# Optimization experiments

Hardware: AMD Instinct MI355X
Metric: run time of the kernel (lower is better)

Reference implementation:

```python
import jax, jax.numpy as jnp
import numpy as np

LN_EPS = 1e-5

def _ln(x, g, b):
    mu = x.mean(-1, keepdims=True)
    var = ((x - mu) ** 2).mean(-1, keepdims=True)
    return (x - mu) * jax.lax.rsqrt(var + LN_EPS) * g + b

def _gru(x, h, wih, whh, bih, bhh):
    # torch GRUCell: gates ordered (r, z, n)
    gi = x @ wih.T + bih
    gh = h @ whh.T + bhh
    ir, iz, inn = jnp.split(gi, 3, axis=-1)
    hr, hz, hn = jnp.split(gh, 3, axis=-1)
    r = jax.nn.sigmoid(ir + hr)
    z = jax.nn.sigmoid(iz + hz)
    n = jnp.tanh(inn + r * hn)
    return (1.0 - z) * n + z * h

def setup_inputs() -> dict:
    key = jax.random.key(0)
    ks = jax.random.split(key, 10)
    B, N, D, S, H = 64, 4096, 128, 8, 256
    w = D ** -0.5  # weight scale to keep activations sane
    return {
        'inputs': jax.random.normal(ks[0], (B, N, D), jnp.float32),
        'slot_noise': jax.random.normal(ks[1], (1, S, D), jnp.float32),
        'slots_mu': jax.random.normal(ks[2], (1, S, D), jnp.float32) * w,
        'slots_log_sigma': jnp.zeros((1, S, D), jnp.float32),
        'wq': jax.random.normal(ks[3], (D, D), jnp.float32) * w,
        'bq': jnp.zeros((D,), jnp.float32),
        'wk': jax.random.normal(ks[4], (D, D), jnp.float32) * w,
        'bk': jnp.zeros((D,), jnp.float32),
        'wv': jax.random.normal(ks[5], (D, D), jnp.float32) * w,
        'bv': jnp.zeros((D,), jnp.float32),
        'gru_wih': jax.random.normal(ks[6], (3 * D, D), jnp.float32) * w,
        'gru_whh': jax.random.normal(ks[7], (3 * D, D), jnp.float32) * w,
        'gru_bih': jnp.zeros((3 * D,), jnp.float32),
        'gru_bhh': jnp.zeros((3 * D,), jnp.float32),
        'ns_g': jnp.ones((D,), jnp.float32),
        'ns_b': jnp.zeros((D,), jnp.float32),
        'ni_g': jnp.ones((D,), jnp.float32),
        'ni_b': jnp.zeros((D,), jnp.float32),
        'mlp_ln_g': jnp.ones((D,), jnp.float32),
        'mlp_ln_b': jnp.zeros((D,), jnp.float32),
        'mlp_w1': jax.random.normal(ks[8], (H, D), jnp.float32) * w,
        'mlp_b1': jnp.zeros((H,), jnp.float32),
        'mlp_w2': jax.random.normal(ks[9], (D, H), jnp.float32) * (H ** -0.5),
        'mlp_b2': jnp.zeros((D,), jnp.float32),
    }

N_ITERS = 3

def reference(inputs, slot_noise, slots_mu, slots_log_sigma, wq, bq, wk, bk, wv, bv,
              gru_wih, gru_whh, gru_bih, gru_bhh, ns_g, ns_b, ni_g, ni_b,
              mlp_ln_g, mlp_ln_b, mlp_w1, mlp_b1, mlp_w2, mlp_b2):
    B, N, D = inputs.shape
    S = slots_mu.shape[1]
    slots = slots_mu + jnp.exp(slots_log_sigma) * slot_noise  # [1,S,D]
    slots = jnp.broadcast_to(slots, (B, S, D))
    x = _ln(inputs, ni_g, ni_b)
    k = x @ wk.T + bk  # [B,N,D]
    v = x @ wv.T + bv
    scale = 1.0 / jnp.sqrt(jnp.float32(D))
    for _ in range(N_ITERS):
        q = _ln(slots, ns_g, ns_b) @ wq.T + bq  # [B,S,D]
        logits = jnp.einsum('bnd,bsd->bns', k, q) * scale
        attn = jax.nn.softmax(logits, axis=-1)  # softmax over slots
        attn_norm = jnp.clip(attn.sum(axis=1, keepdims=True), 1e-8, None)
        slot_attn = attn / attn_norm
        updates = jnp.einsum('bns,bnd->bsd', slot_attn, v)
        slots = _gru(updates, slots, gru_wih, gru_whh, gru_bih, gru_bhh)
        h = jax.nn.gelu(_ln(slots, mlp_ln_g, mlp_ln_b) @ mlp_w1.T + mlp_b1, approximate=False)
        slots = slots + (h @ mlp_w2.T + mlp_b2)
    return slots
```

## Files before the change

kernel.cpp:

```cpp
#include <hip/hip_runtime.h>
#include <hip/hip_bf16.h>
#include <math.h>

#define Bn 64
#define Nn 4096
#define Dn 128
#define Sn 8
#define Hn 256
#define LN_EPS 1e-5f
#define QSCALE 0.08838834764831845f
#define NCHUNK 16

typedef __bf16 bf16x8 __attribute__((ext_vector_type(8)));
typedef float f32x4 __attribute__((ext_vector_type(4)));
typedef unsigned short ushort_t;

__device__ __forceinline__ float dot4(float4 a, float4 b) {
    return a.x*b.x + a.y*b.y + a.z*b.z + a.w*b.w;
}
__device__ __forceinline__ ushort_t f2bf(float f) {
    __bf16 b = (__bf16)f;
    ushort_t u; __builtin_memcpy(&u, &b, 2); return u;
}
__device__ __forceinline__ bf16x8 zero8() {
    bf16x8 z;
    #pragma unroll
    for (int i = 0; i < 8; ++i) z[i] = (__bf16)0.0f;
    return z;
}

__global__ void k_prep(const float* __restrict__ wk, const float* __restrict__ wv,
                       ushort_t* __restrict__ wallT,
                       const float* __restrict__ mu, const float* __restrict__ ls,
                       const float* __restrict__ noise, float* __restrict__ slots) {
    if (blockIdx.x < 128) {
        int o = blockIdx.x * 256 + threadIdx.x;
        int e = o & 7;
        int l = (o >> 3) & 15;
        int q = (o >> 7) & 3;
        int k = (o >> 9) & 3;
        int G = o >> 11;
        int row = G * 16 + l;
        int col = k * 32 + q * 8 + e;
        float f = (row < 128) ? wk[row * 128 + col] : wv[(row - 128) * 128 + col];
        wallT[o] = f2bf(f);
    } else {
        int i = (blockIdx.x - 128) * 256 + threadIdx.x;
        if (i < Sn * Dn) {
            float v = mu[i] + __expf(ls[i]) * noise[i];
            #pragma unroll 4
            for (int b = 0; b < Bn; ++b) slots[b * Sn * Dn + i] = v;
        }
    }
}

__global__ __launch_bounds__(512) void k_lnkv_mfma(
    const float* __restrict__ inp, const float* __restrict__ ni_g, const float* __restrict__ ni_b,
    const ushort_t* __restrict__ wallT, const float* __restrict__ bk, const float* __restrict__ bv,
    ushort_t* __restrict__ kout, ushort_t* __restrict__ vout)
{
    __shared__ ushort_t wsh[32768];
    const int t = threadIdx.x;
    const int lane = t & 63;
    const int w = t >> 6;
    const int l15 = lane & 15, q = lane >> 4;
    const int rowbase = blockIdx.x * 128;
    const int row = rowbase + w * 16 + l15;
    const int b_idx = rowbase >> 12;

    const float* xr = inp + (size_t)row * Dn + q * 8;
    float4 xv[8];
    #pragma unroll
    for (int c = 0; c < 4; ++c) {
        xv[2*c]   = *(const float4*)(xr + c * 32);
        xv[2*c+1] = *(const float4*)(xr + c * 32 + 4);
    }
    #pragma unroll
    for (int i = 0; i < 8; ++i) {
        int off = (i * 512 + t) * 8;
        *(bf16x8*)&wsh[off] = *(const bf16x8*)&wallT[off];
    }

    float s = 0.f, sq = 0.f;
    #pragma unroll
    for (int i = 0; i < 8; ++i) {
        float4 x4 = xv[i];
        s  += x4.x + x4.y + x4.z + x4.w;
        sq += x4.x*x4.x + x4.y*x4.y + x4.z*x4.z + x4.w*x4.w;
    }
    s  += __shfl_xor(s, 16);  s  += __shfl_xor(s, 32);
    sq += __shfl_xor(sq, 16); sq += __shfl_xor(sq, 32);
    float mu = s * (1.0f / 128.0f);
    float rs = rsqrtf(sq * (1.0f / 128.0f) - mu * mu + LN_EPS);

    bf16x8 xf[4];
    #pragma unroll
    for (int c = 0; c < 4; ++c) {
        const float* gp = ni_g + c * 32 + q * 8;
        const float* bp = ni_b + c * 32 + q * 8;
        float4 g0 = *(const float4*)gp, g1 = *(const float4*)(gp + 4);
        float4 b0 = *(const float4*)bp, b1 = *(const float4*)(bp + 4);
        bf16x8 f;
        f[0] = (__bf16)((xv[2*c].x   - mu) * rs * g0.x + b0.x);
        f[1] = (__bf16)((xv[2*c].y   - mu) * rs * g0.y + b0.y);
        f[2] = (__bf16)((xv[2*c].z   - mu) * rs * g0.z + b0.z);
        f[3] = (__bf16)((xv[2*c].w   - mu) * rs * g0.w + b0.w);
        f[4] = (__bf16)((xv[2*c+1].x - mu) * rs * g1.x + b1.x);
        f[5] = (__bf16)((xv[2*c+1].y - mu) * rs * g1.y + b1.y);
        f[6] = (__bf16)((xv[2*c+1].z - mu) * rs * g1.z + b1.z);
        f[7] = (__bf16)((xv[2*c+1].w - mu) * rs * g1.w + b1.w);
        xf[c] = f;
    }

    __syncthreads();

    const int nloc0 = (rowbase & 4095) + w * 16 + q * 4;
    #pragma unroll
    for (int ct = 0; ct < 16; ++ct) {
        bf16x8 af[4];
        #pragma unroll
        for (int k4 = 0; k4 < 4; ++k4)
            af[k4] = *(const bf16x8*)&wsh[((ct * 4 + k4) * 64 + lane) * 8];
        f32x4 acc = {0.f, 0.f, 0.f, 0.f};
        if (ct < 8) {
            #pragma unroll
            for (int k4 = 0; k4 < 4; ++k4)
                acc = __builtin_amdgcn_mfma_f32_16x16x32_bf16(af[k4], xf[k4], acc, 0, 0, 0);
            int d0 = ct * 16 + q * 4;
            float4 bia = *(const float4*)&bk[d0];
            ushort4 o = { f2bf(acc[0] + bia.x), f2bf(acc[1] + bia.y),
                          f2bf(acc[2] + bia.z), f2bf(acc[3] + bia.w) };
            size_t off = ((size_t)(((rowbase >> 4) + w) * 4 + (d0 >> 5)) * 64
                          + ((d0 >> 3) & 3) * 16 + l15) * 8 + (d0 & 7);
            *(ushort4*)&kout[off] = o;
        } else {
            #pragma unroll
            for (int k4 = 0; k4 < 4; ++k4)
                acc = __builtin_amdgcn_mfma_f32_16x16x32_bf16(xf[k4], af[k4], acc, 0, 0, 0);
            int dgrp = ct - 8;
            float bb = bv[dgrp * 16 + l15];
            ushort4 o = { f2bf(acc[0] + bb), f2bf(acc[1] + bb),
                          f2bf(acc[2] + bb), f2bf(acc[3] + bb) };
            size_t off = (((size_t)(b_idx * 8 + dgrp) * 128 + (nloc0 >> 5)) * 64
                          + ((nloc0 >> 3) & 3) * 16 + l15) * 8 + (nloc0 & 7);
            *(ushort4*)&vout[off] = o;
        }
    }
}

__global__ __launch_bounds__(256) void k_qproj2(
    const float* __restrict__ slots, const float* __restrict__ ns_g, const float* __restrict__ ns_b,
    const float* __restrict__ wq, const float* __restrict__ bq,
    ushort_t* __restrict__ qb)
{
    __shared__ float lnq[8][128];
    const int t = threadIdx.x;
    const int bs0 = blockIdx.x * 8;
    {
        int r = t >> 5, c = (t & 31) * 4;
        float4 x4 = *(const float4*)&slots[(size_t)(bs0 + r) * Dn + c];
        float s  = x4.x + x4.y + x4.z + x4.w;
        float sq = x4.x*x4.x + x4.y*x4.y + x4.z*x4.z + x4.w*x4.w;
        #pragma unroll
        for (int m = 1; m <= 16; m <<= 1) { s += __shfl_xor(s, m); sq += __shfl_xor(sq, m); }
        float mu = s * (1.0f / 128.0f);
        float rs = rsqrtf(sq * (1.0f / 128.0f) - mu * mu + LN_EPS);
        lnq[r][c+0] = (x4.x - mu) * rs * ns_g[c+0] + ns_b[c+0];
        lnq[r][c+1] = (x4.y - mu) * rs * ns_g[c+1] + ns_b[c+1];
        lnq[r][c+2] = (x4.z - mu) * rs * ns_g[c+2] + ns_b[c+2];
        lnq[r][c+3] = (x4.w - mu) * rs * ns_g[c+3] + ns_b[c+3];
    }
    __syncthreads();
    {
        int c = t & 127, rb = (t >> 7) * 4;
        const float* W = wq + (size_t)c * Dn;
        float acc[4] = {0.f, 0.f, 0.f, 0.f};
        for (int d = 0; d < 128; d += 4) {
            float4 w4 = *(const float4*)(W + d);
            #pragma unroll
            for (int rr = 0; rr < 4; ++rr) acc[rr] += dot4(w4, *(const float4*)&lnq[rb + rr][d]);
        }
        float bb = bq[c];
        #pragma unroll
        for (int rr = 0; rr < 4; ++rr)
            qb[(size_t)(bs0 + rb + rr) * Dn + c] = f2bf((acc[rr] + bb) * QSCALE);
    }
}

__global__ __launch_bounds__(512) void k_attn_mfma(
    const ushort_t* __restrict__ kbuf, const ushort_t* __restrict__ vtbuf,
    const ushort_t* __restrict__ qb,
    float* __restrict__ upart, float* __restrict__ npart)
{
    __shared__ float ush[8][8][128];
    __shared__ float nsh[8][8];
    __shared__ ushort_t psh[8][8][32];
    const int t = threadIdx.x;
    const int b = blockIdx.y;
    const int chunk = blockIdx.x;
    const int lane = t & 63;
    const int w = t >> 6;
    const int l15 = lane & 15, q = lane >> 4;

    bf16x8 aq[4];
    #pragma unroll
    for (int c = 0; c < 4; ++c) {
        bf16x8 z = zero8();
        if (l15 < 8)
            z = *(const bf16x8*)&qb[((size_t)b * Sn + l15) * Dn + c * 32 + q * 8];
        aq[c] = z;
    }

    const int n32 = chunk * 256 + w * 32;
    const int ng = n32 >> 4;
    const int nc = n32 >> 5;

    f32x4 lg2[2];
    #pragma unroll
    for (int T = 0; T < 2; ++T) {
        f32x4 lg = {0.f, 0.f, 0.f, 0.f};
        #pragma unroll
        for (int c = 0; c < 4; ++c) {
            bf16x8 kf = *(const bf16x8*)&kbuf[(((size_t)b * 256 + ng + T) * 4 + c) * 512 + lane * 8];
            lg = __builtin_amdgcn_mfma_f32_16x16x32_bf16(aq[c], kf, lg, 0, 0, 0);
        }
        lg2[T] = lg;
    }

    bf16x8 bvf[8];
    #pragma unroll
    for (int dg = 0; dg < 8; ++dg)
        bvf[dg] = *(const bf16x8*)&vtbuf[(((size_t)b * 8 + dg) * 128 + nc) * 512 + lane * 8];

    #pragma unroll
    for (int T = 0; T < 2; ++T) {
        f32x4 lg = lg2[T];
        float m = fmaxf(fmaxf(lg[0], lg[1]), fmaxf(lg[2], lg[3]));
        m = fmaxf(m, __shfl_xor(m, 16));
        float e0 = __expf(lg[0] - m);
        float e1 = __expf(lg[1] - m);
        float e2 = __expf(lg[2] - m);
        float e3 = __expf(lg[3] - m);
        float ss = (e0 + e1) + (e2 + e3);
        ss += __shfl_xor(ss, 16);
        float inv = 1.0f / ss;
        if (q < 2) {
            psh[w][q * 4 + 0][T * 16 + l15] = f2bf(e0 * inv);
            psh[w][q * 4 + 1][T * 16 + l15] = f2bf(e1 * inv);
            psh[w][q * 4 + 2][T * 16 + l15] = f2bf(e2 * inv);
            psh[w][q * 4 + 3][T * 16 + l15] = f2bf(e3 * inv);
        }
    }

    bf16x8 pa = zero8();
    if (l15 < 8)
        pa = *(const bf16x8*)&psh[w][l15][q * 8];

    float nacc = 0.f;
    #pragma unroll
    for (int e = 0; e < 8; ++e) nacc += (float)pa[e];

    f32x4 acc[8];
    #pragma unroll
    for (int dg = 0; dg < 8; ++dg) {
        acc[dg] = (f32x4){0.f, 0.f, 0.f, 0.f};
        acc[dg] = __builtin_amdgcn_mfma_f32_16x16x32_bf16(pa, bvf[dg], acc[dg], 0, 0, 0);
    }

    nacc += __shfl_xor(nacc, 16);
    nacc += __shfl_xor(nacc, 32);
    if (lane < 8) nsh[w][lane] = nacc;
    if (q < 2) {
        #pragma unroll
        for (int dg = 0; dg < 8; ++dg)
            #pragma unroll
            for (int r = 0; r < 4; ++r)
                ush[w][q * 4 + r][dg * 16 + l15] = acc[dg][r];
    }
    __syncthreads();
    if (t < 256) {
        int s = t >> 5, d0 = (t & 31) * 4;
        float4 sum = {0.f, 0.f, 0.f, 0.f};
        #pragma unroll
        for (int w8 = 0; w8 < 8; ++w8) {
            float4 vv = *(const float4*)&ush[w8][s][d0];
            sum.x += vv.x; sum.y += vv.y; sum.z += vv.z; sum.w += vv.w;
        }
        *(float4*)&upart[((size_t)chunk * 512 + b * 8 + s) * 128 + d0] = sum;
    }
    if (t < 8) {
        float sn = 0.f;
        #pragma unroll
        for (int w8 = 0; w8 < 8; ++w8) sn += nsh[w8][t];
        npart[chunk * 512 + b * 8 + t] = sn;
    }
}

__global__ __launch_bounds__(256) void k_update3(
    const float* __restrict__ slots,
    const float* __restrict__ upart, const float* __restrict__ npart,
    const float* __restrict__ wih, const float* __restrict__ whh,
    const float* __restrict__ bih, const float* __restrict__ bhh,
    const float* __restrict__ mlg, const float* __restrict__ mlb,
    const float* __restrict__ w1, const float* __restrict__ b1,
    const float* __restrict__ w2, const float* __restrict__ b2,
    const float* __restrict__ ns_g, const float* __restrict__ ns_b,
    const float* __restrict__ wq, const float* __restrict__ bq,
    float* __restrict__ outp, ushort_t* __restrict__ qb, int do_q)
{
    __shared__ float us[128];
    __shared__ float hs[128];
    __shared__ float gs[768];
    __shared__ float hnw[128];
    __shared__ float lns[128];
    __shared__ float h1s[256];
    const int t = threadIdx.x;
    const int bs = blockIdx.x;

    if (t < 128) {
        float u = 0.f;
        #pragma unroll
        for (int c = 0; c < NCHUNK; ++c) u += upart[((size_t)(c * 512 + bs)) * 128 + t];
        float nsum = 0.f;
        #pragma unroll
        for (int c = 0; c < NCHUNK; ++c) nsum += npart[c * 512 + bs];
        us[t] = u / fmaxf(nsum, 1e-8f);
        hs[t] = slots[(size_t)bs * Dn + t];
    }
    __syncthreads();

    #pragma unroll
    for (int jj = 0; jj < 3; ++jj) {
        int j = t + jj * 256;
        const float* W = (j < 384) ? (wih + (size_t)j * Dn) : (whh + (size_t)(j - 384) * Dn);
        const float* X = (j < 384) ? us : hs;
        float a = 0.f;
        #pragma unroll 8
        for (int d = 0; d < 128; d += 4)
            a += dot4(*(const float4*)(W + d), *(const float4*)(X + d));
        gs[j] = a;
    }
    __syncthreads();

    if (t < 64) {
        float hnew[2];
        #pragma unroll
        for (int e = 0; e < 2; ++e) {
            int i = t + e * 64;
            float ir = gs[i]       + bih[i],       hr = gs[384 + i] + bhh[i];
            float iz = gs[128 + i] + bih[128 + i], hz = gs[512 + i] + bhh[128 + i];
            float in_= gs[256 + i] + bih[256 + i], hn = gs[640 + i] + bhh[256 + i];
            float r = 1.0f / (1.0f + __expf(-(ir + hr)));
            float z = 1.0f / (1.0f + __expf(-(iz + hz)));
            float n = tanhf(in_ + r * hn);
            hnew[e] = (1.0f - z) * n + z * hs[i];
        }
        float s  = hnew[0] + hnew[1];
        float sq = hnew[0]*hnew[0] + hnew[1]*hnew[1];
        #pragma unroll
        for (int m = 1; m <= 32; m <<= 1) { s += __shfl_xor(s, m); sq += __shfl_xor(sq, m); }
        float mu = s * (1.0f / 128.0f);
        float rs = rsqrtf(sq * (1.0f / 128.0f) - mu * mu + LN_EPS);
        #pragma unroll
        for (int e = 0; e < 2; ++e) {
            int i = t + e * 64;
            hnw[i] = hnew[e];
            lns[i] = (hnew[e] - mu) * rs * mlg[i] + mlb[i];
        }
    }
    __syncthreads();

    {
        const float* W = w1 + (size_t)t * Dn;
        float a = 0.f;
        #pragma unroll 8
        for (int d = 0; d < 128; d += 4)
            a += dot4(*(const float4*)(W + d), *(const float4*)&lns[d]);
        float x = a + b1[t];
        h1s[t] = 0.5f * x * (1.0f + erff(x * 0.70710678118654752f));
    }
    __syncthreads();

    if (t < 128) {
        const float* W = w2 + (size_t)t * Hn;
        float a = 0.f;
        #pragma unroll 8
        for (int d = 0; d < 256; d += 4)
            a += dot4(*(const float4*)(W + d), *(const float4*)&h1s[d]);
        float o = hnw[t] + a + b2[t];
        outp[(size_t)bs * Dn + t] = o;
        us[t] = o;
    }
    if (do_q) {
        __syncthreads();
        if (t < 64) {
            float v0 = us[t], v1 = us[t + 64];
            float s  = v0 + v1;
            float sq = v0*v0 + v1*v1;
            #pragma unroll
            for (int m = 1; m <= 32; m <<= 1) { s += __shfl_xor(s, m); sq += __shfl_xor(sq, m); }
            float mu = s * (1.0f / 128.0f);
            float rs = rsqrtf(sq * (1.0f / 128.0f) - mu * mu + LN_EPS);
            lns[t]      = (v0 - mu) * rs * ns_g[t]      + ns_b[t];
            lns[t + 64] = (v1 - mu) * rs * ns_g[t + 64] + ns_b[t + 64];
        }
        __syncthreads();
        if (t < 128) {
            const float* W = wq + (size_t)t * Dn;
            float a = 0.f;
            #pragma unroll 8
            for (int d = 0; d < 128; d += 4)
                a += dot4(*(const float4*)(W + d), *(const float4*)&lns[d]);
            qb[(size_t)bs * Dn + t] = f2bf((a + bq[t]) * QSCALE);
        }
    }
}

extern "C" void kernel_launch(void* const* d_in, const int* in_sizes, int n_in,
                              void* d_out, int out_size, void* d_ws, size_t ws_size,
                              hipStream_t stream) {
    (void)in_sizes; (void)n_in; (void)out_size; (void)ws_size;
    const float* inputs   = (const float*)d_in[0];
    const float* noise    = (const float*)d_in[1];
    const float* slots_mu = (const float*)d_in[2];
    const float* slots_ls = (const float*)d_in[3];
    const float* wq  = (const float*)d_in[4];
    const float* bq  = (const float*)d_in[5];
    const float* wk  = (const float*)d_in[6];
    const float* bk  = (const float*)d_in[7];
    const float* wv  = (const float*)d_in[8];
    const float* bv  = (const float*)d_in[9];
    const float* gwih = (const float*)d_in[10];
    const float* gwhh = (const float*)d_in[11];
    const float* gbih = (const float*)d_in[12];
    const float* gbhh = (const float*)d_in[13];
    const float* ns_g = (const float*)d_in[14];
    const float* ns_b = (const float*)d_in[15];
    const float* ni_g = (const float*)d_in[16];
    const float* ni_b = (const float*)d_in[17];
    const float* mlg  = (const float*)d_in[18];
    const float* mlb  = (const float*)d_in[19];
    const float* mw1  = (const float*)d_in[20];
    const float* mb1  = (const float*)d_in[21];
    const float* mw2  = (const float*)d_in[22];
    const float* mb2  = (const float*)d_in[23];

    float* ws      = (float*)d_ws;
    float* slots   = ws;
    float* upart   = ws + 65536;
    float* npart   = ws + 1114112;
    ushort_t* qb    = (ushort_t*)(ws + 1122304);
    ushort_t* wallT = (ushort_t*)(ws + 1155072);
    ushort_t* kbuf  = (ushort_t*)(ws + 1171456);
    ushort_t* vtbuf = kbuf + 33554432;

    k_prep<<<132, 256, 0, stream>>>(wk, wv, wallT, slots_mu, slots_ls, noise, slots);
    k_lnkv_mfma<<<2048, 512, 0, stream>>>(inputs, ni_g, ni_b, wallT, bk, bv, kbuf, vtbuf);
    k_qproj2<<<64, 256, 0, stream>>>(slots, ns_g, ns_b, wq, bq, qb);
    for (int iter = 0; iter < 3; ++iter) {
        k_attn_mfma<<<dim3(NCHUNK, 64), 512, 0, stream>>>(kbuf, vtbuf, qb, upart, npart);
        float* outp = (iter == 2) ? (float*)d_out : slots;
        k_update3<<<512, 256, 0, stream>>>(slots, upart, npart, gwih, gwhh, gbih, gbhh,
                                           mlg, mlb, mw1, mb1, mw2, mb2, ns_g, ns_b, wq, bq,
                                           outp, qb, (iter == 2) ? 0 : 1);
    }
}
```

Measured before the change: 464.1 us.

## Fuse attention and slot-update iterations into one persistent kernel with grid barriers

```diff
diff --git a/kernel.cpp b/kernel.cpp
--- a/kernel.cpp
+++ b/kernel.cpp
@@ -9,7 +9,7 @@
 #define Hn 256
 #define LN_EPS 1e-5f
 #define QSCALE 0.08838834764831845f
-#define NCHUNK 16
+#define NCHUNK 4
 
 typedef __bf16 bf16x8 __attribute__((ext_vector_type(8)));
 typedef float f32x4 __attribute__((ext_vector_type(4)));
@@ -32,7 +32,9 @@
 __global__ void k_prep(const float* __restrict__ wk, const float* __restrict__ wv,
                        ushort_t* __restrict__ wallT,
                        const float* __restrict__ mu, const float* __restrict__ ls,
-                       const float* __restrict__ noise, float* __restrict__ slots) {
+                       const float* __restrict__ noise, float* __restrict__ slots,
+                       unsigned* __restrict__ barcnt) {
+    if (blockIdx.x == 128 && threadIdx.x == 0) *barcnt = 0u;
     if (blockIdx.x < 128) {
         int o = blockIdx.x * 256 + threadIdx.x;
         int e = o & 7;
@@ -187,118 +189,23 @@
     }
 }
 
-__global__ __launch_bounds__(512) void k_attn_mfma(
+__device__ __forceinline__ void gridbar(unsigned* cnt, unsigned target) {
+    __syncthreads();
+    if (threadIdx.x == 0) {
+        __threadfence();
+        atomicAdd(cnt, 1u);
+        while (atomicAdd(cnt, 0u) < target)
+            __builtin_amdgcn_s_sleep(16);
+        __threadfence();
+    }
+    __syncthreads();
+}
+
+__global__ __launch_bounds__(512) void k_iter(
     const ushort_t* __restrict__ kbuf, const ushort_t* __restrict__ vtbuf,
-    const ushort_t* __restrict__ qb,
-    float* __restrict__ upart, float* __restrict__ npart)
-{
-    __shared__ float ush[8][8][128];
-    __shared__ float nsh[8][8];
-    __shared__ ushort_t psh[8][8][32];
-    const int t = threadIdx.x;
-    const int b = blockIdx.y;
-    const int chunk = blockIdx.x;
-    const int lane = t & 63;
-    const int w = t >> 6;
-    const int l15 = lane & 15, q = lane >> 4;
-
-    bf16x8 aq[4];
-    #pragma unroll
-    for (int c = 0; c < 4; ++c) {
-        bf16x8 z = zero8();
-        if (l15 < 8)
-            z = *(const bf16x8*)&qb[((size_t)b * Sn + l15) * Dn + c * 32 + q * 8];
-        aq[c] = z;
-    }
-
-    const int n32 = chunk * 256 + w * 32;
-    const int ng = n32 >> 4;
-    const int nc = n32 >> 5;
-
-    f32x4 lg2[2];
-    #pragma unroll
-    for (int T = 0; T < 2; ++T) {
-        f32x4 lg = {0.f, 0.f, 0.f, 0.f};
-        #pragma unroll
-        for (int c = 0; c < 4; ++c) {
-            bf16x8 kf = *(const bf16x8*)&kbuf[(((size_t)b * 256 + ng + T) * 4 + c) * 512 + lane * 8];
-            lg = __builtin_amdgcn_mfma_f32_16x16x32_bf16(aq[c], kf, lg, 0, 0, 0);
-        }
-        lg2[T] = lg;
-    }
-
-    bf16x8 bvf[8];
-    #pragma unroll
-    for (int dg = 0; dg < 8; ++dg)
-        bvf[dg] = *(const bf16x8*)&vtbuf[(((size_t)b * 8 + dg) * 128 + nc) * 512 + lane * 8];
-
-    #pragma unroll
-    for (int T = 0; T < 2; ++T) {
-        f32x4 lg = lg2[T];
-        float m = fmaxf(fmaxf(lg[0], lg[1]), fmaxf(lg[2], lg[3]));
-        m = fmaxf(m, __shfl_xor(m, 16));
-        float e0 = __expf(lg[0] - m);
-        float e1 = __expf(lg[1] - m);
-        float e2 = __expf(lg[2] - m);
-        float e3 = __expf(lg[3] - m);
-        float ss = (e0 + e1) + (e2 + e3);
-        ss += __shfl_xor(ss, 16);
-        float inv = 1.0f / ss;
-        if (q < 2) {
-            psh[w][q * 4 + 0][T * 16 + l15] = f2bf(e0 * inv);
-            psh[w][q * 4 + 1][T * 16 + l15] = f2bf(e1 * inv);
-            psh[w][q * 4 + 2][T * 16 + l15] = f2bf(e2 * inv);
-            psh[w][q * 4 + 3][T * 16 + l15] = f2bf(e3 * inv);
-        }
-    }
-
-    bf16x8 pa = zero8();
-    if (l15 < 8)
-        pa = *(const bf16x8*)&psh[w][l15][q * 8];
-
-    float nacc = 0.f;
-    #pragma unroll
-    for (int e = 0; e < 8; ++e) nacc += (float)pa[e];
-
-    f32x4 acc[8];
-    #pragma unroll
-    for (int dg = 0; dg < 8; ++dg) {
-        acc[dg] = (f32x4){0.f, 0.f, 0.f, 0.f};
-        acc[dg] = __builtin_amdgcn_mfma_f32_16x16x32_bf16(pa, bvf[dg], acc[dg], 0, 0, 0);
-    }
-
-    nacc += __shfl_xor(nacc, 16);
-    nacc += __shfl_xor(nacc, 32);
-    if (lane < 8) nsh[w][lane] = nacc;
-    if (q < 2) {
-        #pragma unroll
-        for (int dg = 0; dg < 8; ++dg)
-            #pragma unroll
-            for (int r = 0; r < 4; ++r)
-                ush[w][q * 4 + r][dg * 16 + l15] = acc[dg][r];
-    }
-    __syncthreads();
-    if (t < 256) {
-        int s = t >> 5, d0 = (t & 31) * 4;
-        float4 sum = {0.f, 0.f, 0.f, 0.f};
-        #pragma unroll
-        for (int w8 = 0; w8 < 8; ++w8) {
-            float4 vv = *(const float4*)&ush[w8][s][d0];
-            sum.x += vv.x; sum.y += vv.y; sum.z += vv.z; sum.w += vv.w;
-        }
-        *(float4*)&upart[((size_t)chunk * 512 + b * 8 + s) * 128 + d0] = sum;
-    }
-    if (t < 8) {
-        float sn = 0.f;
-        #pragma unroll
-        for (int w8 = 0; w8 < 8; ++w8) sn += nsh[w8][t];
-        npart[chunk * 512 + b * 8 + t] = sn;
-    }
-}
-
-__global__ __launch_bounds__(256) void k_update3(
-    const float* __restrict__ slots,
-    const float* __restrict__ upart, const float* __restrict__ npart,
+    ushort_t* __restrict__ qbA, ushort_t* __restrict__ qbB,
+    float* __restrict__ slots,
+    float* __restrict__ upart, float* __restrict__ npart,
     const float* __restrict__ wih, const float* __restrict__ whh,
     const float* __restrict__ bih, const float* __restrict__ bhh,
     const float* __restrict__ mlg, const float* __restrict__ mlb,
@@ -306,113 +213,238 @@
     const float* __restrict__ w2, const float* __restrict__ b2,
     const float* __restrict__ ns_g, const float* __restrict__ ns_b,
     const float* __restrict__ wq, const float* __restrict__ bq,
-    float* __restrict__ outp, ushort_t* __restrict__ qb, int do_q)
+    float* __restrict__ outp, unsigned* __restrict__ barcnt)
 {
-    __shared__ float us[128];
-    __shared__ float hs[128];
-    __shared__ float gs[768];
-    __shared__ float hnw[128];
-    __shared__ float lns[128];
-    __shared__ float h1s[256];
+    __shared__ float ush[8][8][128];
+    __shared__ float nsh[8][8];
+    __shared__ ushort_t psh[8][8][32];
+    __shared__ float us2[2][128], hs2[2][128], gs2[2][768];
+    __shared__ float hnw2[2][128], lns2[2][128], h1s2[2][256];
+
     const int t = threadIdx.x;
-    const int bs = blockIdx.x;
-
-    if (t < 128) {
-        float u = 0.f;
-        #pragma unroll
-        for (int c = 0; c < NCHUNK; ++c) u += upart[((size_t)(c * 512 + bs)) * 128 + t];
-        float nsum = 0.f;
-        #pragma unroll
-        for (int c = 0; c < NCHUNK; ++c) nsum += npart[c * 512 + bs];
-        us[t] = u / fmaxf(nsum, 1e-8f);
-        hs[t] = slots[(size_t)bs * Dn + t];
-    }
-    __syncthreads();
-
-    #pragma unroll
-    for (int jj = 0; jj < 3; ++jj) {
-        int j = t + jj * 256;
-        const float* W = (j < 384) ? (wih + (size_t)j * Dn) : (whh + (size_t)(j - 384) * Dn);
-        const float* X = (j < 384) ? us : hs;
-        float a = 0.f;
-        #pragma unroll 8
-        for (int d = 0; d < 128; d += 4)
-            a += dot4(*(const float4*)(W + d), *(const float4*)(X + d));
-        gs[j] = a;
-    }
-    __syncthreads();
-
-    if (t < 64) {
-        float hnew[2];
-        #pragma unroll
-        for (int e = 0; e < 2; ++e) {
-            int i = t + e * 64;
-            float ir = gs[i]       + bih[i],       hr = gs[384 + i] + bhh[i];
-            float iz = gs[128 + i] + bih[128 + i], hz = gs[512 + i] + bhh[128 + i];
-            float in_= gs[256 + i] + bih[256 + i], hn = gs[640 + i] + bhh[256 + i];
-            float r = 1.0f / (1.0f + __expf(-(ir + hr)));
-            float z = 1.0f / (1.0f + __expf(-(iz + hz)));
-            float n = tanhf(in_ + r * hn);
-            hnew[e] = (1.0f - z) * n + z * hs[i];
+    const int blk = blockIdx.x;
+    const int lane = t & 63;
+    const int w = t >> 6;
+    const int l15 = lane & 15, q = lane >> 4;
+    const int b = blk & 63;
+    const int ch = blk >> 6;
+
+    unsigned bars = 0;
+
+    for (int iter = 0; iter < 3; ++iter) {
+        const ushort_t* qcur = (iter == 1) ? qbB : qbA;
+        ushort_t* qnxt = (iter == 0) ? qbB : qbA;
+        float* up = upart + (size_t)iter * (NCHUNK * 512 * 128);
+        float* np = npart + (size_t)iter * (NCHUNK * 512);
+        const int do_q = (iter < 2);
+
+        {
+            bf16x8 aq[4];
+            #pragma unroll
+            for (int c = 0; c < 4; ++c) {
+                bf16x8 z = zero8();
+                if (l15 < 8)
+                    z = *(const bf16x8*)&qcur[((size_t)b * Sn + l15) * Dn + c * 32 + q * 8];
+                aq[c] = z;
+            }
+
+            f32x4 acc[8];
+            #pragma unroll
+            for (int dg = 0; dg < 8; ++dg) acc[dg] = (f32x4){0.f, 0.f, 0.f, 0.f};
+            float nacc = 0.f;
+
+            for (int k = 0; k < 4; ++k) {
+                const int n32 = ch * 1024 + w * 128 + k * 32;
+                const int ng = n32 >> 4;
+                const int nc = n32 >> 5;
+
+                f32x4 lg2[2];
+                #pragma unroll
+                for (int T = 0; T < 2; ++T) {
+                    f32x4 lg = {0.f, 0.f, 0.f, 0.f};
+                    #pragma unroll
+                    for (int c = 0; c < 4; ++c) {
+                        bf16x8 kf = *(const bf16x8*)&kbuf[(((size_t)b * 256 + ng + T) * 4 + c) * 512 + lane * 8];
+                        lg = __builtin_amdgcn_mfma_f32_16x16x32_bf16(aq[c], kf, lg, 0, 0, 0);
+                    }
+                    lg2[T] = lg;
+                }
+
+                bf16x8 bvf[8];
+                #pragma unroll
+                for (int dg = 0; dg < 8; ++dg)
+                    bvf[dg] = *(const bf16x8*)&vtbuf[(((size_t)b * 8 + dg) * 128 + nc) * 512 + lane * 8];
+
+                #pragma unroll
+                for (int T = 0; T < 2; ++T) {
+                    f32x4 lg = lg2[T];
+                    float m = fmaxf(fmaxf(lg[0], lg[1]), fmaxf(lg[2], lg[3]));
+                    m = fmaxf(m, __shfl_xor(m, 16));
+                    float e0 = __expf(lg[0] - m);
+                    float e1 = __expf(lg[1] - m);
+                    float e2 = __expf(lg[2] - m);
+                    float e3 = __expf(lg[3] - m);
+                    float ss = (e0 + e1) + (e2 + e3);
+                    ss += __shfl_xor(ss, 16);
+                    float inv = 1.0f / ss;
+                    if (q < 2) {
+                        psh[w][q * 4 + 0][T * 16 + l15] = f2bf(e0 * inv);
+                        psh[w][q * 4 + 1][T * 16 + l15] = f2bf(e1 * inv);
+                        psh[w][q * 4 + 2][T * 16 + l15] = f2bf(e2 * inv);
+                        psh[w][q * 4 + 3][T * 16 + l15] = f2bf(e3 * inv);
+                    }
+                }
+
+                bf16x8 pa = zero8();
+                if (l15 < 8)
+                    pa = *(const bf16x8*)&psh[w][l15][q * 8];
+
+                #pragma unroll
+                for (int e = 0; e < 8; ++e) nacc += (float)pa[e];
+
+                #pragma unroll
+                for (int dg = 0; dg < 8; ++dg)
+                    acc[dg] = __builtin_amdgcn_mfma_f32_16x16x32_bf16(pa, bvf[dg], acc[dg], 0, 0, 0);
+            }
+
+            nacc += __shfl_xor(nacc, 16);
+            nacc += __shfl_xor(nacc, 32);
+            if (lane < 8) nsh[w][lane] = nacc;
+            if (q < 2) {
+                #pragma unroll
+                for (int dg = 0; dg < 8; ++dg)
+                    #pragma unroll
+                    for (int r = 0; r < 4; ++r)
+                        ush[w][q * 4 + r][dg * 16 + l15] = acc[dg][r];
+            }
+            __syncthreads();
+            if (t < 256) {
+                int s = t >> 5, d0 = (t & 31) * 4;
+                float4 sum = {0.f, 0.f, 0.f, 0.f};
+                #pragma unroll
+                for (int w8 = 0; w8 < 8; ++w8) {
+                    float4 vv = *(const float4*)&ush[w8][s][d0];
+                    sum.x += vv.x; sum.y += vv.y; sum.z += vv.z; sum.w += vv.w;
+                }
+                *(float4*)&up[((size_t)ch * 512 + b * 8 + s) * 128 + d0] = sum;
+            }
+            if (t < 8) {
+                float sn = 0.f;
+                #pragma unroll
+                for (int w8 = 0; w8 < 8; ++w8) sn += nsh[w8][t];
+                np[ch * 512 + b * 8 + t] = sn;
+            }
         }
-        float s  = hnew[0] + hnew[1];
-        float sq = hnew[0]*hnew[0] + hnew[1]*hnew[1];
-        #pragma unroll
-        for (int m = 1; m <= 32; m <<= 1) { s += __shfl_xor(s, m); sq += __shfl_xor(sq, m); }
-        float mu = s * (1.0f / 128.0f);
-        float rs = rsqrtf(sq * (1.0f / 128.0f) - mu * mu + LN_EPS);
-        #pragma unroll
-        for (int e = 0; e < 2; ++e) {
-            int i = t + e * 64;
-            hnw[i] = hnew[e];
-            lns[i] = (hnew[e] - mu) * rs * mlg[i] + mlb[i];
+
+        gridbar(barcnt, (++bars) * 256);
+
+        {
+            const int half = t >> 8;
+            const int tl = t & 255;
+            const int bs = blk * 2 + half;
+            float* usU = us2[half]; float* hsU = hs2[half]; float* gsU = gs2[half];
+            float* hnwU = hnw2[half]; float* lnsU = lns2[half]; float* h1sU = h1s2[half];
+            float* oout = (iter == 2) ? outp : slots;
+
+            if (tl < 128) {
+                float u = 0.f, nsum = 0.f;
+                #pragma unroll
+                for (int c = 0; c < NCHUNK; ++c) u += up[((size_t)(c * 512 + bs)) * 128 + tl];
+                #pragma unroll
+                for (int c = 0; c < NCHUNK; ++c) nsum += np[c * 512 + bs];
+                usU[tl] = u / fmaxf(nsum, 1e-8f);
+                hsU[tl] = slots[(size_t)bs * Dn + tl];
+            }
+            __syncthreads();
+
+            #pragma unroll
+            for (int jj = 0; jj < 3; ++jj) {
+                int j = tl + jj * 256;
+                const float* W = (j < 384) ? (wih + (size_t)j * Dn) : (whh + (size_t)(j - 384) * Dn);
+                const float* X = (j < 384) ? usU : hsU;
+                float a = 0.f;
+                #pragma unroll 8
+                for (int d = 0; d < 128; d += 4)
+                    a += dot4(*(const float4*)(W + d), *(const float4*)(X + d));
+                gsU[j] = a;
+            }
+            __syncthreads();
+
+            if (tl < 64) {
+                float hnew[2];
+                #pragma unroll
+                for (int e = 0; e < 2; ++e) {
+                    int i = tl + e * 64;
+                    float ir = gsU[i]       + bih[i],       hr = gsU[384 + i] + bhh[i];
+                    float iz = gsU[128 + i] + bih[128 + i], hz = gsU[512 + i] + bhh[128 + i];
+                    float in_= gsU[256 + i] + bih[256 + i], hn = gsU[640 + i] + bhh[256 + i];
+                    float r = 1.0f / (1.0f + __expf(-(ir + hr)));
+                    float z = 1.0f / (1.0f + __expf(-(iz + hz)));
+                    float n = tanhf(in_ + r * hn);
+                    hnew[e] = (1.0f - z) * n + z * hsU[i];
+                }
+                float s  = hnew[0] + hnew[1];
+                float sq = hnew[0]*hnew[0] + hnew[1]*hnew[1];
+                #pragma unroll
+                for (int m = 1; m <= 32; m <<= 1) { s += __shfl_xor(s, m); sq += __shfl_xor(sq, m); }
+                float mu = s * (1.0f / 128.0f);
+                float rs = rsqrtf(sq * (1.0f / 128.0f) - mu * mu + LN_EPS);
+                #pragma unroll
+                for (int e = 0; e < 2; ++e) {
+                    int i = tl + e * 64;
+                    hnwU[i] = hnew[e];
+                    lnsU[i] = (hnew[e] - mu) * rs * mlg[i] + mlb[i];
+                }
+            }
+            __syncthreads();
+
+            {
+                const float* W = w1 + (size_t)tl * Dn;
+                float a = 0.f;
+                #pragma unroll 8
+                for (int d = 0; d < 128; d += 4)
+                    a += dot4(*(const float4*)(W + d), *(const float4*)&lnsU[d]);
+                float x = a + b1[tl];
+                h1sU[tl] = 0.5f * x * (1.0f + erff(x * 0.70710678118654752f));
+            }
+            __syncthreads();
+
+            if (tl < 128) {
+                const float* W = w2 + (size_t)tl * Hn;
+                float a = 0.f;
+                #pragma unroll 8
+                for (int d = 0; d < 256; d += 4)
+                    a += dot4(*(const float4*)(W + d), *(const float4*)&h1sU[d]);
+                float o = hnwU[tl] + a + b2[tl];
+                oout[(size_t)bs * Dn + tl] = o;
+                usU[tl] = o;
+            }
+            if (do_q) {
+                __syncthreads();
+                if (tl < 64) {
+                    float v0 = usU[tl], v1 = usU[tl + 64];
+                    float s  = v0 + v1;
+                    float sq = v0*v0 + v1*v1;
+                    #pragma unroll
+                    for (int m = 1; m <= 32; m <<= 1) { s += __shfl_xor(s, m); sq += __shfl_xor(sq, m); }
+                    float mu = s * (1.0f / 128.0f);
+                    float rs = rsqrtf(sq * (1.0f / 128.0f) - mu * mu + LN_EPS);
+                    lnsU[tl]      = (v0 - mu) * rs * ns_g[tl]      + ns_b[tl];
+                    lnsU[tl + 64] = (v1 - mu) * rs * ns_g[tl + 64] + ns_b[tl + 64];
+                }
+                __syncthreads();
+                if (tl < 128) {
+                    const float* W = wq + (size_t)tl * Dn;
+                    float a = 0.f;
+                    #pragma unroll 8
+                    for (int d = 0; d < 128; d += 4)
+                        a += dot4(*(const float4*)(W + d), *(const float4*)&lnsU[d]);
+                    qnxt[(size_t)bs * Dn + tl] = f2bf((a + bq[tl]) * QSCALE);
+                }
+            }
         }
-    }
-    __syncthreads();
-
-    {
-        const float* W = w1 + (size_t)t * Dn;
-        float a = 0.f;
-        #pragma unroll 8
-        for (int d = 0; d < 128; d += 4)
-            a += dot4(*(const float4*)(W + d), *(const float4*)&lns[d]);
-        float x = a + b1[t];
-        h1s[t] = 0.5f * x * (1.0f + erff(x * 0.70710678118654752f));
-    }
-    __syncthreads();
-
-    if (t < 128) {
-        const float* W = w2 + (size_t)t * Hn;
-        float a = 0.f;
-        #pragma unroll 8
-        for (int d = 0; d < 256; d += 4)
-            a += dot4(*(const float4*)(W + d), *(const float4*)&h1s[d]);
-        float o = hnw[t] + a + b2[t];
-        outp[(size_t)bs * Dn + t] = o;
-        us[t] = o;
-    }
-    if (do_q) {
-        __syncthreads();
-        if (t < 64) {
-            float v0 = us[t], v1 = us[t + 64];
-            float s  = v0 + v1;
-            float sq = v0*v0 + v1*v1;
-            #pragma unroll
-            for (int m = 1; m <= 32; m <<= 1) { s += __shfl_xor(s, m); sq += __shfl_xor(sq, m); }
-            float mu = s * (1.0f / 128.0f);
-            float rs = rsqrtf(sq * (1.0f / 128.0f) - mu * mu + LN_EPS);
-            lns[t]      = (v0 - mu) * rs * ns_g[t]      + ns_b[t];
-            lns[t + 64] = (v1 - mu) * rs * ns_g[t + 64] + ns_b[t + 64];
-        }
-        __syncthreads();
-        if (t < 128) {
-            const float* W = wq + (size_t)t * Dn;
-            float a = 0.f;
-            #pragma unroll 8
-            for (int d = 0; d < 128; d += 4)
-                a += dot4(*(const float4*)(W + d), *(const float4*)&lns[d]);
-            qb[(size_t)bs * Dn + t] = f2bf((a + bq[t]) * QSCALE);
-        }
+
+        if (iter < 2) gridbar(barcnt, (++bars) * 256);
     }
 }
 
@@ -448,20 +480,19 @@
     float* ws      = (float*)d_ws;
     float* slots   = ws;
     float* upart   = ws + 65536;
-    float* npart   = ws + 1114112;
-    ushort_t* qb    = (ushort_t*)(ws + 1122304);
-    ushort_t* wallT = (ushort_t*)(ws + 1155072);
-    ushort_t* kbuf  = (ushort_t*)(ws + 1171456);
+    float* npart   = ws + 851968;
+    ushort_t* qbA   = (ushort_t*)(ws + 858112);
+    ushort_t* qbB   = (ushort_t*)(ws + 874496);
+    ushort_t* wallT = (ushort_t*)(ws + 890880);
+    unsigned* barcnt = (unsigned*)(ws + 907264);
+    ushort_t* kbuf  = (ushort_t*)(ws + 907776);
     ushort_t* vtbuf = kbuf + 33554432;
 
-    k_prep<<<132, 256, 0, stream>>>(wk, wv, wallT, slots_mu, slots_ls, noise, slots);
+    k_prep<<<132, 256, 0, stream>>>(wk, wv, wallT, slots_mu, slots_ls, noise, slots, barcnt);
     k_lnkv_mfma<<<2048, 512, 0, stream>>>(inputs, ni_g, ni_b, wallT, bk, bv, kbuf, vtbuf);
-    k_qproj2<<<64, 256, 0, stream>>>(slots, ns_g, ns_b, wq, bq, qb);
-    for (int iter = 0; iter < 3; ++iter) {
-        k_attn_mfma<<<dim3(NCHUNK, 64), 512, 0, stream>>>(kbuf, vtbuf, qb, upart, npart);
-        float* outp = (iter == 2) ? (float*)d_out : slots;
-        k_update3<<<512, 256, 0, stream>>>(slots, upart, npart, gwih, gwhh, gbih, gbhh,
-                                           mlg, mlb, mw1, mb1, mw2, mb2, ns_g, ns_b, wq, bq,
-                                           outp, qb, (iter == 2) ? 0 : 1);
-    }
-}
+    k_qproj2<<<64, 256, 0, stream>>>(slots, ns_g, ns_b, wq, bq, qbA);
+    k_iter<<<256, 512, 0, stream>>>(kbuf, vtbuf, qbA, qbB, slots, upart, npart,
+                                    gwih, gwhh, gbih, gbhh, mlg, mlb, mw1, mb1,
+                                    mw2, mb2, ns_g, ns_b, wq, bq,
+                                    (float*)d_out, barcnt);
+}
```

Result: slower. 533.1 us (+14.9%).
